# Optimization experiments

Measured on AMD Instinct MI355X. Metric: run time of the kernel, lower is better.

The kernel has to match this reference:

```python
import jax, jax.numpy as jnp
import numpy as np

B, S, C, H, D = 4, 2048, 512, 8, 64
EPS = 1e-5
SCALE = D ** -0.5


def layer_norm(x, w, b):
    m = jnp.mean(x, axis=-1, keepdims=True)
    v = jnp.var(x, axis=-1, keepdims=True)
    return (x - m) * jax.lax.rsqrt(v + EPS) * w + b


def setup_inputs() -> dict:
    key = jax.random.key(0)
    ks = jax.random.split(key, 7)
    s = 0.02
    return {
        "x": jax.random.normal(ks[0], (B, S, C), jnp.float32),
        "Wq": jax.random.normal(ks[1], (C, H * D), jnp.float32) * s,
        "Wk": jax.random.normal(ks[2], (C, H * D), jnp.float32) * s,
        "Wv": jax.random.normal(ks[3], (C, H * D), jnp.float32) * s,
        "Wo": jax.random.normal(ks[4], (H * D, C), jnp.float32) * s,
        "ln1_w": jnp.ones((C,), jnp.float32), "ln1_b": jnp.zeros((C,), jnp.float32),
        "ff_ln1_w": jnp.ones((C,), jnp.float32), "ff_ln1_b": jnp.zeros((C,), jnp.float32),
        "ff_w1": jax.random.normal(ks[5], (C, C), jnp.float32) * s, "ff_b1": jnp.zeros((C,), jnp.float32),
        "ff_ln2_w": jnp.ones((C,), jnp.float32), "ff_ln2_b": jnp.zeros((C,), jnp.float32),
        "ff_w2": jax.random.normal(ks[6], (C, C), jnp.float32) * s, "ff_b2": jnp.zeros((C,), jnp.float32),
        "ln2_w": jnp.ones((C,), jnp.float32), "ln2_b": jnp.zeros((C,), jnp.float32),
    }


def causal_attention(x, Wq, Wk, Wv, Wo):
    # Mathematically identical to the bucketed memory-efficient attention:
    # online-softmax bucketing changes compute order, not the result.
    q = (x @ Wq).reshape(B, S, H, D).transpose(0, 2, 1, 3)  # [B,H,S,D]
    k = (x @ Wk).reshape(B, S, H, D).transpose(0, 2, 1, 3)
    v = (x @ Wv).reshape(B, S, H, D).transpose(0, 2, 1, 3)
    scores = jnp.einsum('bhqd,bhkd->bhqk', q, k) * SCALE  # [B,H,S,S]
    causal = jnp.tril(jnp.ones((S, S), bool))
    scores = jnp.where(causal, scores, jnp.finfo(scores.dtype).min)
    attn = jax.nn.softmax(scores, axis=-1)
    out = jnp.einsum('bhqk,bhkd->bhqd', attn, v)
    out = out.transpose(0, 2, 1, 3).reshape(B, S, H * D)
    return out @ Wo


def reference(x, Wq, Wk, Wv, Wo, ln1_w, ln1_b, ff_ln1_w, ff_ln1_b, ff_w1, ff_b1,
              ff_ln2_w, ff_ln2_b, ff_w2, ff_b2, ln2_w, ln2_b):
    a = causal_attention(x, Wq, Wk, Wv, Wo)
    x_ln = layer_norm(a + x, ln1_w, ln1_b)
    h = layer_norm(x_ln, ff_ln1_w, ff_ln1_b) @ ff_w1 + ff_b1
    h = layer_norm(h, ff_ln2_w, ff_ln2_b) @ ff_w2 + ff_b2
    return layer_norm(h + x_ln, ln2_w, ln2_b)
```

## Files before the change

kernel.cpp:

```cpp
#include <hip/hip_runtime.h>

#define B_ 4
#define S_ 2048
#define C_ 512
#define H_ 8
#define D_ 64
#define M_ 8192

typedef short s8v __attribute__((ext_vector_type(8)));
typedef short s4v __attribute__((ext_vector_type(4)));
typedef float f4v __attribute__((ext_vector_type(4)));
typedef unsigned short u16;
typedef unsigned int u32;

__device__ __forceinline__ u16 f2b(float f) {
    u32 u = __builtin_bit_cast(u32, f);
    u = u + 0x7fffu + ((u >> 16) & 1u);
    return (u16)(u >> 16);
}

__device__ __forceinline__ void gl2lds16(const void* g, void* l) {
    __builtin_amdgcn_global_load_lds(
        (const __attribute__((address_space(1))) void*)g,
        (__attribute__((address_space(3))) void*)l, 16, 0, 0);
}

__global__ __launch_bounds__(256) void conv_k(const float* __restrict__ s,
                                              u16* __restrict__ d) {
    const int i = (blockIdx.x * 256 + threadIdx.x) * 4;
    const float4 v = *(const float4*)&s[i];
    ushort4 o;
    o.x = f2b(v.x); o.y = f2b(v.y); o.z = f2b(v.z); o.w = f2b(v.w);
    *(ushort4*)&d[i] = o;
}

__global__ __launch_bounds__(256) void trconv6_k(const float* __restrict__ s0,
                                                 const float* __restrict__ s1,
                                                 const float* __restrict__ s2,
                                                 const float* __restrict__ s3,
                                                 const float* __restrict__ s4,
                                                 const float* __restrict__ s5,
                                                 u16* __restrict__ d0,
                                                 u16* __restrict__ d1,
                                                 u16* __restrict__ d2,
                                                 u16* __restrict__ d3,
                                                 u16* __restrict__ d4,
                                                 u16* __restrict__ d5)
{
    const float* W; u16* Wt;
    switch (blockIdx.z) {
        case 0: W = s0; Wt = d0; break;
        case 1: W = s1; Wt = d1; break;
        case 2: W = s2; Wt = d2; break;
        case 3: W = s3; Wt = d3; break;
        case 4: W = s4; Wt = d4; break;
        default: W = s5; Wt = d5; break;
    }
    __shared__ float t[32][33];
    const int tx = threadIdx.x & 31, ty = threadIdx.x >> 5;
    const int n0 = blockIdx.x * 32, k0 = blockIdx.y * 32;
    #pragma unroll
    for (int i = 0; i < 4; ++i)
        t[ty + i * 8][tx] = W[(size_t)(k0 + ty + i * 8) * C_ + n0 + tx];
    __syncthreads();
    #pragma unroll
    for (int i = 0; i < 4; ++i)
        Wt[(size_t)(n0 + ty + i * 8) * C_ + k0 + tx] = f2b(t[tx][ty + i * 8]);
}

template <bool OB>
__global__ __launch_bounds__(256) void gemm_k(const u16* __restrict__ A,
                                              const u16* __restrict__ Bt,
                                              const float* __restrict__ bias,
                                              void* __restrict__ outv)
{
    __shared__ u16 As[2][4][16][32];
    __shared__ u16 Bs[2][4][16][32];
    const int tid = threadIdx.x;
    const int lane = tid & 63, w = tid >> 6;
    const int q4 = lane >> 4, l16 = lane & 15;
    const int wr = w >> 1, wc = w & 1;
    const int bm = blockIdx.y * 64, bn = blockIdx.x * 64;
    const int lr = lane >> 2, lc = (lane & 3) * 8;

    f4v acc[2][2];
    #pragma unroll
    for (int i = 0; i < 2; ++i)
        #pragma unroll
        for (int j = 0; j < 2; ++j) acc[i][j] = (f4v){0.f, 0.f, 0.f, 0.f};

    gl2lds16(A  + (size_t)(bm + w * 16 + lr) * C_ + lc, (char*)As + w * 1024);
    gl2lds16(Bt + (size_t)(bn + w * 16 + lr) * C_ + lc, (char*)Bs + w * 1024);

    for (int kt = 0; kt < 16; ++kt) {
        __syncthreads();
        const int buf = kt & 1;
        if (kt < 15) {
            const int nb = buf ^ 1, k0 = (kt + 1) * 32;
            gl2lds16(A  + (size_t)(bm + w * 16 + lr) * C_ + k0 + lc,
                     (char*)As + nb * 4096 + w * 1024);
            gl2lds16(Bt + (size_t)(bn + w * 16 + lr) * C_ + k0 + lc,
                     (char*)Bs + nb * 4096 + w * 1024);
        }
        s8v a[2], bfr[2];
        #pragma unroll
        for (int i = 0; i < 2; ++i) {
            const int row = wr * 32 + i * 16 + l16;
            a[i] = *(const s8v*)&As[buf][row >> 4][row & 15][q4 * 8];
        }
        #pragma unroll
        for (int j = 0; j < 2; ++j) {
            const int row = wc * 32 + j * 16 + l16;
            bfr[j] = *(const s8v*)&Bs[buf][row >> 4][row & 15][q4 * 8];
        }
        #pragma unroll
        for (int i = 0; i < 2; ++i)
            #pragma unroll
            for (int j = 0; j < 2; ++j)
                acc[i][j] = __builtin_amdgcn_mfma_f32_16x16x32_bf16(a[i], bfr[j], acc[i][j], 0, 0, 0);
    }

    #pragma unroll
    for (int j = 0; j < 2; ++j) {
        const int n = bn + wc * 32 + j * 16 + l16;
        const float bj = bias ? bias[n] : 0.0f;
        #pragma unroll
        for (int i = 0; i < 2; ++i) {
            const int m = bm + wr * 32 + i * 16 + q4 * 4;
            #pragma unroll
            for (int reg = 0; reg < 4; ++reg) {
                const float vv = acc[i][j][reg] + bj;
                if constexpr (OB) ((u16*)outv)[(size_t)(m + reg) * C_ + n] = f2b(vv);
                else              ((float*)outv)[(size_t)(m + reg) * C_ + n] = vv;
            }
        }
    }
}

__global__ __launch_bounds__(256) void qkv_k(const u16* __restrict__ A,
                                             const u16* __restrict__ Wq,
                                             const u16* __restrict__ Wk,
                                             const u16* __restrict__ Wv,
                                             u16* __restrict__ oq,
                                             u16* __restrict__ ok,
                                             u16* __restrict__ ovt)
{
    __shared__ u16 As[2][4][16][32];
    __shared__ u16 Bs[2][4][16][32];
    const int tid = threadIdx.x;
    const int lane = tid & 63, w = tid >> 6;
    const int q4 = lane >> 4, l16 = lane & 15;
    const int wr = w >> 1, wc = w & 1;
    const int nt = blockIdx.x, which = nt >> 3;
    const u16* Bt = which == 0 ? Wq : (which == 1 ? Wk : Wv);
    const int bm = blockIdx.y * 64, bn = (nt & 7) * 64;
    const int lr = lane >> 2, lc = (lane & 3) * 8;

    f4v acc[2][2];
    #pragma unroll
    for (int i = 0; i < 2; ++i)
        #pragma unroll
        for (int j = 0; j < 2; ++j) acc[i][j] = (f4v){0.f, 0.f, 0.f, 0.f};

    gl2lds16(A  + (size_t)(bm + w * 16 + lr) * C_ + lc, (char*)As + w * 1024);
    gl2lds16(Bt + (size_t)(bn + w * 16 + lr) * C_ + lc, (char*)Bs + w * 1024);

    for (int kt = 0; kt < 16; ++kt) {
        __syncthreads();
        const int buf = kt & 1;
        if (kt < 15) {
            const int nb = buf ^ 1, k0 = (kt + 1) * 32;
            gl2lds16(A  + (size_t)(bm + w * 16 + lr) * C_ + k0 + lc,
                     (char*)As + nb * 4096 + w * 1024);
            gl2lds16(Bt + (size_t)(bn + w * 16 + lr) * C_ + k0 + lc,
                     (char*)Bs + nb * 4096 + w * 1024);
        }
        s8v a[2], bfr[2];
        #pragma unroll
        for (int i = 0; i < 2; ++i) {
            const int row = wr * 32 + i * 16 + l16;
            a[i] = *(const s8v*)&As[buf][row >> 4][row & 15][q4 * 8];
        }
        #pragma unroll
        for (int j = 0; j < 2; ++j) {
            const int row = wc * 32 + j * 16 + l16;
            bfr[j] = *(const s8v*)&Bs[buf][row >> 4][row & 15][q4 * 8];
        }
        #pragma unroll
        for (int i = 0; i < 2; ++i)
            #pragma unroll
            for (int j = 0; j < 2; ++j)
                acc[i][j] = __builtin_amdgcn_mfma_f32_16x16x32_bf16(a[i], bfr[j], acc[i][j], 0, 0, 0);
    }

    if (which != 2) {
        u16* outp = which == 0 ? oq : ok;
        #pragma unroll
        for (int j = 0; j < 2; ++j) {
            const int n = bn + wc * 32 + j * 16 + l16;
            #pragma unroll
            for (int i = 0; i < 2; ++i) {
                const int m = bm + wr * 32 + i * 16 + q4 * 4;
                #pragma unroll
                for (int reg = 0; reg < 4; ++reg)
                    outp[(size_t)(m + reg) * C_ + n] = f2b(acc[i][j][reg]);
            }
        }
    } else {
        const int bglob = bm >> 11;
        const int sbase = bm & (S_ - 1);
        #pragma unroll
        for (int j = 0; j < 2; ++j) {
            const int n = bn + wc * 32 + j * 16 + l16;
            const int h = n >> 6, d = n & 63;
            u16* vrow = ovt + ((size_t)(bglob * H_ + h) * D_ + d) * S_;
            const int xw = d & 7;
            #pragma unroll
            for (int i = 0; i < 2; ++i) {
                const int s = sbase + wr * 32 + i * 16 + q4 * 4;
                const int pg = ((s & 31) >> 2) ^ xw;
                s4v pv;
                #pragma unroll
                for (int reg = 0; reg < 4; ++reg) pv[reg] = (short)f2b(acc[i][j][reg]);
                *(s4v*)&vrow[(s & ~31) + (pg << 2)] = pv;
            }
        }
    }
}

template <bool OB>
__global__ __launch_bounds__(256) void ln_k(const float* __restrict__ in,
                                            const float* __restrict__ res,
                                            const float* __restrict__ w,
                                            const float* __restrict__ bb,
                                            void* __restrict__ outv)
{
    const int lane = threadIdx.x & 63;
    const int row  = blockIdx.x * 4 + (threadIdx.x >> 6);
    const float* p = in + (size_t)row * C_;
    float4 v0 = *(const float4*)&p[lane * 4];
    float4 v1 = *(const float4*)&p[256 + lane * 4];
    if (res) {
        const float* rp = res + (size_t)row * C_;
        const float4 r0 = *(const float4*)&rp[lane * 4];
        const float4 r1 = *(const float4*)&rp[256 + lane * 4];
        v0.x += r0.x; v0.y += r0.y; v0.z += r0.z; v0.w += r0.w;
        v1.x += r1.x; v1.y += r1.y; v1.z += r1.z; v1.w += r1.w;
    }
    float s  = v0.x + v0.y + v0.z + v0.w + v1.x + v1.y + v1.z + v1.w;
    float ss = v0.x*v0.x + v0.y*v0.y + v0.z*v0.z + v0.w*v0.w
             + v1.x*v1.x + v1.y*v1.y + v1.z*v1.z + v1.w*v1.w;
    #pragma unroll
    for (int off = 32; off >= 1; off >>= 1) {
        s  += __shfl_xor(s, off);
        ss += __shfl_xor(ss, off);
    }
    const float mean = s * (1.0f / C_);
    const float var  = ss * (1.0f / C_) - mean * mean;
    const float rstd = rsqrtf(var + 1e-5f);

    const float4 w0 = *(const float4*)&w[lane * 4];
    const float4 w1 = *(const float4*)&w[256 + lane * 4];
    const float4 b0 = *(const float4*)&bb[lane * 4];
    const float4 b1 = *(const float4*)&bb[256 + lane * 4];
    float4 o0, o1;
    o0.x = (v0.x - mean) * rstd * w0.x + b0.x;
    o0.y = (v0.y - mean) * rstd * w0.y + b0.y;
    o0.z = (v0.z - mean) * rstd * w0.z + b0.z;
    o0.w = (v0.w - mean) * rstd * w0.w + b0.w;
    o1.x = (v1.x - mean) * rstd * w1.x + b1.x;
    o1.y = (v1.y - mean) * rstd * w1.y + b1.y;
    o1.z = (v1.z - mean) * rstd * w1.z + b1.z;
    o1.w = (v1.w - mean) * rstd * w1.w + b1.w;
    if constexpr (OB) {
        u16* op = (u16*)outv + (size_t)row * C_;
        ushort4 u0, u1;
        u0.x = f2b(o0.x); u0.y = f2b(o0.y); u0.z = f2b(o0.z); u0.w = f2b(o0.w);
        u1.x = f2b(o1.x); u1.y = f2b(o1.y); u1.z = f2b(o1.z); u1.w = f2b(o1.w);
        *(ushort4*)&op[lane * 4]       = u0;
        *(ushort4*)&op[256 + lane * 4] = u1;
    } else {
        float* op = (float*)outv + (size_t)row * C_;
        *(float4*)&op[lane * 4]       = o0;
        *(float4*)&op[256 + lane * 4] = o1;
    }
}

__global__ __launch_bounds__(256) void ln2x_k(const float* __restrict__ in,
                                              const float* __restrict__ res,
                                              const float* __restrict__ w1,
                                              const float* __restrict__ b1,
                                              const float* __restrict__ w2,
                                              const float* __restrict__ b2,
                                              float* __restrict__ out1,
                                              u16* __restrict__ out2)
{
    const int lane = threadIdx.x & 63;
    const int row  = blockIdx.x * 4 + (threadIdx.x >> 6);
    const float* p  = in  + (size_t)row * C_;
    const float* rp = res + (size_t)row * C_;
    float4 v0 = *(const float4*)&p[lane * 4];
    float4 v1 = *(const float4*)&p[256 + lane * 4];
    {
        const float4 r0 = *(const float4*)&rp[lane * 4];
        const float4 r1 = *(const float4*)&rp[256 + lane * 4];
        v0.x += r0.x; v0.y += r0.y; v0.z += r0.z; v0.w += r0.w;
        v1.x += r1.x; v1.y += r1.y; v1.z += r1.z; v1.w += r1.w;
    }
    float s  = v0.x + v0.y + v0.z + v0.w + v1.x + v1.y + v1.z + v1.w;
    float ss = v0.x*v0.x + v0.y*v0.y + v0.z*v0.z + v0.w*v0.w
             + v1.x*v1.x + v1.y*v1.y + v1.z*v1.z + v1.w*v1.w;
    #pragma unroll
    for (int off = 32; off >= 1; off >>= 1) {
        s  += __shfl_xor(s, off);
        ss += __shfl_xor(ss, off);
    }
    float mean = s * (1.0f / C_);
    float var  = ss * (1.0f / C_) - mean * mean;
    float rstd = rsqrtf(var + 1e-5f);

    const float4 wA0 = *(const float4*)&w1[lane * 4];
    const float4 wA1 = *(const float4*)&w1[256 + lane * 4];
    const float4 bA0 = *(const float4*)&b1[lane * 4];
    const float4 bA1 = *(const float4*)&b1[256 + lane * 4];
    float4 y0, y1v;
    y0.x  = (v0.x - mean) * rstd * wA0.x + bA0.x;
    y0.y  = (v0.y - mean) * rstd * wA0.y + bA0.y;
    y0.z  = (v0.z - mean) * rstd * wA0.z + bA0.z;
    y0.w  = (v0.w - mean) * rstd * wA0.w + bA0.w;
    y1v.x = (v1.x - mean) * rstd * wA1.x + bA1.x;
    y1v.y = (v1.y - mean) * rstd * wA1.y + bA1.y;
    y1v.z = (v1.z - mean) * rstd * wA1.z + bA1.z;
    y1v.w = (v1.w - mean) * rstd * wA1.w + bA1.w;
    float* op1 = out1 + (size_t)row * C_;
    *(float4*)&op1[lane * 4]       = y0;
    *(float4*)&op1[256 + lane * 4] = y1v;

    s  = y0.x + y0.y + y0.z + y0.w + y1v.x + y1v.y + y1v.z + y1v.w;
    ss = y0.x*y0.x + y0.y*y0.y + y0.z*y0.z + y0.w*y0.w
       + y1v.x*y1v.x + y1v.y*y1v.y + y1v.z*y1v.z + y1v.w*y1v.w;
    #pragma unroll
    for (int off = 32; off >= 1; off >>= 1) {
        s  += __shfl_xor(s, off);
        ss += __shfl_xor(ss, off);
    }
    mean = s * (1.0f / C_);
    var  = ss * (1.0f / C_) - mean * mean;
    rstd = rsqrtf(var + 1e-5f);

    const float4 wB0 = *(const float4*)&w2[lane * 4];
    const float4 wB1 = *(const float4*)&w2[256 + lane * 4];
    const float4 bB0 = *(const float4*)&b2[lane * 4];
    const float4 bB1 = *(const float4*)&b2[256 + lane * 4];
    ushort4 u0, u1;
    u0.x = f2b((y0.x - mean) * rstd * wB0.x + bB0.x);
    u0.y = f2b((y0.y - mean) * rstd * wB0.y + bB0.y);
    u0.z = f2b((y0.z - mean) * rstd * wB0.z + bB0.z);
    u0.w = f2b((y0.w - mean) * rstd * wB0.w + bB0.w);
    u1.x = f2b((y1v.x - mean) * rstd * wB1.x + bB1.x);
    u1.y = f2b((y1v.y - mean) * rstd * wB1.y + bB1.y);
    u1.z = f2b((y1v.z - mean) * rstd * wB1.z + bB1.z);
    u1.w = f2b((y1v.w - mean) * rstd * wB1.w + bB1.w);
    u16* op2 = out2 + (size_t)row * C_;
    *(ushort4*)&op2[lane * 4]       = u0;
    *(ushort4*)&op2[256 + lane * 4] = u1;
}

__global__ __launch_bounds__(256) void attn_k(const u16* __restrict__ Q,
                                              const u16* __restrict__ K,
                                              const u16* __restrict__ Vt,
                                              u16* __restrict__ O)
{
    __shared__ u16 Ks[2][2][64][32];
    __shared__ u16 Vs[2][2][64][32];
    const int tid = threadIdx.x;
    const int lane = tid & 63, w = tid >> 6;
    const int q4 = lane >> 4, l16 = lane & 15;
    const int x = blockIdx.x, h = blockIdx.y, b = blockIdx.z;
    const int qb = (x & 1) ? 31 - (x >> 1) : (x >> 1);
    const size_t base  = ((size_t)b * S_) * C_ + h * D_;
    const size_t basev = ((size_t)(b * H_ + h)) * D_ * S_;
    const int lr = lane >> 2, lc = (lane & 3) * 8;

    s8v qf[2];
    #pragma unroll
    for (int kh = 0; kh < 2; ++kh)
        qf[kh] = *(const s8v*)&Q[base + (size_t)(qb * 64 + w * 16 + l16) * C_ + kh * 32 + q4 * 8];

    #pragma unroll
    for (int r = 0; r < 2; ++r) {
        const int seg = r * 4 + w;
        const int row = (seg & 3) * 16 + lr;
        const int kh = seg >> 2;
        gl2lds16(K  + base  + (size_t)row * C_ + kh * 32 + lc, (char*)Ks + seg * 1024);
        gl2lds16(Vt + basev + (size_t)row * S_ + kh * 32 + lc, (char*)Vs + seg * 1024);
    }

    f4v o[4];
    float lp[4] = {0.f, 0.f, 0.f, 0.f};
    #pragma unroll
    for (int j = 0; j < 4; ++j) o[j] = (f4v){0.f, 0.f, 0.f, 0.f};

    const int qrow = w * 16 + l16;
    for (int kb = 0; kb <= qb; ++kb) {
        __syncthreads();
        const int buf = kb & 1;
        if (kb < qb) {
            const int nb = buf ^ 1, kn = kb + 1;
            #pragma unroll
            for (int r = 0; r < 2; ++r) {
                const int seg = r * 4 + w;
                const int row = (seg & 3) * 16 + lr;
                const int kh = seg >> 2;
                gl2lds16(K  + base  + (size_t)(kn * 64 + row) * C_ + kh * 32 + lc,
                         (char*)Ks + nb * 8192 + seg * 1024);
                gl2lds16(Vt + basev + (size_t)row * S_ + kn * 64 + kh * 32 + lc,
                         (char*)Vs + nb * 8192 + seg * 1024);
            }
        }

        f4v sc[4];
        #pragma unroll
        for (int j = 0; j < 4; ++j) sc[j] = (f4v){0.f, 0.f, 0.f, 0.f};
        #pragma unroll
        for (int kh = 0; kh < 2; ++kh) {
            #pragma unroll
            for (int j = 0; j < 4; ++j) {
                const s8v kf = *(const s8v*)&Ks[buf][kh][j * 16 + l16][q4 * 8];
                sc[j] = __builtin_amdgcn_mfma_f32_16x16x32_bf16(kf, qf[kh], sc[j], 0, 0, 0);
            }
        }

        const bool diag = (kb == qb);
        s4v pa[4];
        #pragma unroll
        for (int j = 0; j < 4; ++j) {
            float ps = 0.0f;
            #pragma unroll
            for (int reg = 0; reg < 4; ++reg) {
                float t = fmaf(sc[j][reg], 0.18033688011112043f, -11.541560327111707f);
                if (diag && (j * 16 + q4 * 4 + reg) > qrow) t = -128.0f;
                const float p = exp2f(t);
                ps += p;
                pa[j][reg] = (short)(__builtin_bit_cast(u32, p) >> 16);
            }
            lp[j] += ps;
        }

        #pragma unroll
        for (int c = 0; c < 4; ++c) {
            const int gh = (((c & 1) * 4 + q4) ^ (l16 & 7)) * 4;
            #pragma unroll
            for (int dj = 0; dj < 4; ++dj) {
                const s4v vb = *(const s4v*)&Vs[buf][c >> 1][dj * 16 + l16][gh];
                o[dj] = __builtin_amdgcn_mfma_f32_16x16x16bf16_1k(pa[c], vb, o[dj], 0, 0, 0);
            }
        }
    }

    float lt = (lp[0] + lp[1]) + (lp[2] + lp[3]);
    lt += __shfl_xor(lt, 16);
    lt += __shfl_xor(lt, 32);
    #pragma unroll
    for (int reg = 0; reg < 4; ++reg) {
        const float inv = 1.0f / __shfl(lt, q4 * 4 + reg);
        const size_t rowoff = base + (size_t)(qb * 64 + w * 16 + q4 * 4 + reg) * C_;
        #pragma unroll
        for (int dj = 0; dj < 4; ++dj)
            O[rowoff + dj * 16 + l16] = f2b(o[dj][reg] * inv);
    }
}

extern "C" void kernel_launch(void* const* d_in, const int* in_sizes, int n_in,
                              void* d_out, int out_size, void* d_ws, size_t ws_size,
                              hipStream_t stream)
{
    const float* x       = (const float*)d_in[0];
    const float* Wq      = (const float*)d_in[1];
    const float* Wk      = (const float*)d_in[2];
    const float* Wv      = (const float*)d_in[3];
    const float* Wo      = (const float*)d_in[4];
    const float* ln1_w   = (const float*)d_in[5];
    const float* ln1_b   = (const float*)d_in[6];
    const float* ffln1_w = (const float*)d_in[7];
    const float* ffln1_b = (const float*)d_in[8];
    const float* ff_w1   = (const float*)d_in[9];
    const float* ff_b1   = (const float*)d_in[10];
    const float* ffln2_w = (const float*)d_in[11];
    const float* ffln2_b = (const float*)d_in[12];
    const float* ff_w2   = (const float*)d_in[13];
    const float* ff_b2   = (const float*)d_in[14];
    const float* ln2_w   = (const float*)d_in[15];
    const float* ln2_b   = (const float*)d_in[16];
    float* out = (float*)d_out;

    const size_t MC = (size_t)M_ * C_;
    const size_t WW = (size_t)C_ * C_;
    u16* xb   = (u16*)d_ws;
    u16* WqT  = xb + MC;
    u16* WkT  = WqT + WW;
    u16* WvT  = WkT + WW;
    u16* WoT  = WvT + WW;
    u16* W1T  = WoT + WW;
    u16* W2T  = W1T + WW;
    u16* qbuf = W2T + WW;
    u16* kbuf = qbuf + MC;
    u16* vbuf = kbuf + MC;
    u16* vtbuf= vbuf + MC;
    u16*  abuf = xb;
    float* tf  = (float*)qbuf;
    float* xln = (float*)vbuf;

    const dim3 gg(C_ / 64, M_ / 64);
    const dim3 gq(24, M_ / 64);
    const dim3 ga(32, H_, B_);
    const dim3 gt(16, 16, 6);
    const int  gl = M_ / 4;

    conv_k<<<MC / 1024, 256, 0, stream>>>(x, xb);
    trconv6_k<<<gt, 256, 0, stream>>>(Wq, Wk, Wv, Wo, ff_w1, ff_w2,
                                      WqT, WkT, WvT, WoT, W1T, W2T);

    qkv_k<<<gq, 256, 0, stream>>>(xb, WqT, WkT, WvT, qbuf, kbuf, vtbuf);
    attn_k<<<ga, 256, 0, stream>>>(qbuf, kbuf, vtbuf, abuf);

    gemm_k<false><<<gg, 256, 0, stream>>>(abuf, WoT, nullptr, tf);
    ln2x_k<<<gl, 256, 0, stream>>>(tf, x, ln1_w, ln1_b, ffln1_w, ffln1_b,
                                   xln, xb);
    gemm_k<false><<<gg, 256, 0, stream>>>(xb, W1T, ff_b1, tf);
    ln_k<true><<<gl, 256, 0, stream>>>(tf, nullptr, ffln2_w, ffln2_b, xb);
    gemm_k<false><<<gg, 256, 0, stream>>>(xb, W2T, ff_b2, tf);
    ln_k<false><<<gl, 256, 0, stream>>>(tf, xln, ln2_w, ln2_b, out);
}
```

Measured before the change: 267.6 us.

## Store GEMM and LayerNorm intermediates in bf16 and swizzle K layout

```diff
diff --git a/kernel.cpp b/kernel.cpp
--- a/kernel.cpp
+++ b/kernel.cpp
@@ -17,6 +17,12 @@
     u32 u = __builtin_bit_cast(u32, f);
     u = u + 0x7fffu + ((u >> 16) & 1u);
     return (u16)(u >> 16);
+}
+
+__device__ __forceinline__ void b2f8(const s8v v, float* f) {
+    #pragma unroll
+    for (int k = 0; k < 8; ++k)
+        f[k] = __builtin_bit_cast(float, (u32)(u16)v[k] << 16);
 }
 
 __device__ __forceinline__ void gl2lds16(const void* g, void* l) {
@@ -193,8 +199,7 @@
                 acc[i][j] = __builtin_amdgcn_mfma_f32_16x16x32_bf16(a[i], bfr[j], acc[i][j], 0, 0, 0);
     }
 
-    if (which != 2) {
-        u16* outp = which == 0 ? oq : ok;
+    if (which == 0) {
         #pragma unroll
         for (int j = 0; j < 2; ++j) {
             const int n = bn + wc * 32 + j * 16 + l16;
@@ -203,7 +208,20 @@
                 const int m = bm + wr * 32 + i * 16 + q4 * 4;
                 #pragma unroll
                 for (int reg = 0; reg < 4; ++reg)
-                    outp[(size_t)(m + reg) * C_ + n] = f2b(acc[i][j][reg]);
+                    oq[(size_t)(m + reg) * C_ + n] = f2b(acc[i][j][reg]);
+            }
+        }
+    } else if (which == 1) {
+        #pragma unroll
+        for (int j = 0; j < 2; ++j) {
+            const int n = bn + wc * 32 + j * 16 + l16;
+            const int nswz = (n & ~31) | ((((n >> 3) & 3) ^ q4) << 3) | (n & 7);
+            #pragma unroll
+            for (int i = 0; i < 2; ++i) {
+                const int m = bm + wr * 32 + i * 16 + q4 * 4;
+                #pragma unroll
+                for (int reg = 0; reg < 4; ++reg)
+                    ok[(size_t)(m + reg) * C_ + nswz] = f2b(acc[i][j][reg]);
             }
         }
     } else {
@@ -228,142 +246,138 @@
     }
 }
 
-template <bool OB>
-__global__ __launch_bounds__(256) void ln_k(const float* __restrict__ in,
-                                            const float* __restrict__ res,
-                                            const float* __restrict__ w,
-                                            const float* __restrict__ bb,
-                                            void* __restrict__ outv)
+__global__ __launch_bounds__(256) void ln2xb_k(const u16* __restrict__ in,
+                                               const float* __restrict__ res,
+                                               const float* __restrict__ w1,
+                                               const float* __restrict__ b1,
+                                               const float* __restrict__ w2,
+                                               const float* __restrict__ b2,
+                                               u16* __restrict__ out1,
+                                               u16* __restrict__ out2)
 {
     const int lane = threadIdx.x & 63;
     const int row  = blockIdx.x * 4 + (threadIdx.x >> 6);
-    const float* p = in + (size_t)row * C_;
-    float4 v0 = *(const float4*)&p[lane * 4];
-    float4 v1 = *(const float4*)&p[256 + lane * 4];
-    if (res) {
-        const float* rp = res + (size_t)row * C_;
-        const float4 r0 = *(const float4*)&rp[lane * 4];
-        const float4 r1 = *(const float4*)&rp[256 + lane * 4];
-        v0.x += r0.x; v0.y += r0.y; v0.z += r0.z; v0.w += r0.w;
-        v1.x += r1.x; v1.y += r1.y; v1.z += r1.z; v1.w += r1.w;
-    }
-    float s  = v0.x + v0.y + v0.z + v0.w + v1.x + v1.y + v1.z + v1.w;
-    float ss = v0.x*v0.x + v0.y*v0.y + v0.z*v0.z + v0.w*v0.w
-             + v1.x*v1.x + v1.y*v1.y + v1.z*v1.z + v1.w*v1.w;
-    #pragma unroll
-    for (int off = 32; off >= 1; off >>= 1) {
-        s  += __shfl_xor(s, off);
-        ss += __shfl_xor(ss, off);
-    }
-    const float mean = s * (1.0f / C_);
-    const float var  = ss * (1.0f / C_) - mean * mean;
-    const float rstd = rsqrtf(var + 1e-5f);
-
-    const float4 w0 = *(const float4*)&w[lane * 4];
-    const float4 w1 = *(const float4*)&w[256 + lane * 4];
-    const float4 b0 = *(const float4*)&bb[lane * 4];
-    const float4 b1 = *(const float4*)&bb[256 + lane * 4];
-    float4 o0, o1;
-    o0.x = (v0.x - mean) * rstd * w0.x + b0.x;
-    o0.y = (v0.y - mean) * rstd * w0.y + b0.y;
-    o0.z = (v0.z - mean) * rstd * w0.z + b0.z;
-    o0.w = (v0.w - mean) * rstd * w0.w + b0.w;
-    o1.x = (v1.x - mean) * rstd * w1.x + b1.x;
-    o1.y = (v1.y - mean) * rstd * w1.y + b1.y;
-    o1.z = (v1.z - mean) * rstd * w1.z + b1.z;
-    o1.w = (v1.w - mean) * rstd * w1.w + b1.w;
-    if constexpr (OB) {
-        u16* op = (u16*)outv + (size_t)row * C_;
-        ushort4 u0, u1;
-        u0.x = f2b(o0.x); u0.y = f2b(o0.y); u0.z = f2b(o0.z); u0.w = f2b(o0.w);
-        u1.x = f2b(o1.x); u1.y = f2b(o1.y); u1.z = f2b(o1.z); u1.w = f2b(o1.w);
-        *(ushort4*)&op[lane * 4]       = u0;
-        *(ushort4*)&op[256 + lane * 4] = u1;
-    } else {
-        float* op = (float*)outv + (size_t)row * C_;
-        *(float4*)&op[lane * 4]       = o0;
-        *(float4*)&op[256 + lane * 4] = o1;
-    }
-}
-
-__global__ __launch_bounds__(256) void ln2x_k(const float* __restrict__ in,
-                                              const float* __restrict__ res,
-                                              const float* __restrict__ w1,
-                                              const float* __restrict__ b1,
-                                              const float* __restrict__ w2,
-                                              const float* __restrict__ b2,
-                                              float* __restrict__ out1,
-                                              u16* __restrict__ out2)
+    const size_t off = (size_t)row * C_ + lane * 8;
+    float v[8];
+    b2f8(*(const s8v*)&in[off], v);
+    {
+        const float4 r0 = *(const float4*)&res[off];
+        const float4 r1 = *(const float4*)&res[off + 4];
+        v[0] += r0.x; v[1] += r0.y; v[2] += r0.z; v[3] += r0.w;
+        v[4] += r1.x; v[5] += r1.y; v[6] += r1.z; v[7] += r1.w;
+    }
+    float s = 0.f, ss = 0.f;
+    #pragma unroll
+    for (int k = 0; k < 8; ++k) { s += v[k]; ss += v[k] * v[k]; }
+    #pragma unroll
+    for (int o = 32; o >= 1; o >>= 1) { s += __shfl_xor(s, o); ss += __shfl_xor(ss, o); }
+    float mean = s * (1.0f / C_);
+    float rstd = rsqrtf(ss * (1.0f / C_) - mean * mean + 1e-5f);
+
+    const float4 wA0 = *(const float4*)&w1[lane * 8];
+    const float4 wA1 = *(const float4*)&w1[lane * 8 + 4];
+    const float4 bA0 = *(const float4*)&b1[lane * 8];
+    const float4 bA1 = *(const float4*)&b1[lane * 8 + 4];
+    const float wA[8] = {wA0.x, wA0.y, wA0.z, wA0.w, wA1.x, wA1.y, wA1.z, wA1.w};
+    const float bA[8] = {bA0.x, bA0.y, bA0.z, bA0.w, bA1.x, bA1.y, bA1.z, bA1.w};
+    float y[8];
+    s8v o1;
+    #pragma unroll
+    for (int k = 0; k < 8; ++k) {
+        y[k] = (v[k] - mean) * rstd * wA[k] + bA[k];
+        o1[k] = (short)f2b(y[k]);
+    }
+    *(s8v*)&out1[off] = o1;
+
+    s = 0.f; ss = 0.f;
+    #pragma unroll
+    for (int k = 0; k < 8; ++k) { s += y[k]; ss += y[k] * y[k]; }
+    #pragma unroll
+    for (int o = 32; o >= 1; o >>= 1) { s += __shfl_xor(s, o); ss += __shfl_xor(ss, o); }
+    mean = s * (1.0f / C_);
+    rstd = rsqrtf(ss * (1.0f / C_) - mean * mean + 1e-5f);
+
+    const float4 wB0 = *(const float4*)&w2[lane * 8];
+    const float4 wB1 = *(const float4*)&w2[lane * 8 + 4];
+    const float4 bB0 = *(const float4*)&b2[lane * 8];
+    const float4 bB1 = *(const float4*)&b2[lane * 8 + 4];
+    const float wB[8] = {wB0.x, wB0.y, wB0.z, wB0.w, wB1.x, wB1.y, wB1.z, wB1.w};
+    const float bB[8] = {bB0.x, bB0.y, bB0.z, bB0.w, bB1.x, bB1.y, bB1.z, bB1.w};
+    s8v o2;
+    #pragma unroll
+    for (int k = 0; k < 8; ++k)
+        o2[k] = (short)f2b((y[k] - mean) * rstd * wB[k] + bB[k]);
+    *(s8v*)&out2[off] = o2;
+}
+
+__global__ __launch_bounds__(256) void lnb_k(const u16* __restrict__ in,
+                                             const float* __restrict__ w,
+                                             const float* __restrict__ bb,
+                                             u16* __restrict__ out)
 {
     const int lane = threadIdx.x & 63;
     const int row  = blockIdx.x * 4 + (threadIdx.x >> 6);
-    const float* p  = in  + (size_t)row * C_;
-    const float* rp = res + (size_t)row * C_;
-    float4 v0 = *(const float4*)&p[lane * 4];
-    float4 v1 = *(const float4*)&p[256 + lane * 4];
-    {
-        const float4 r0 = *(const float4*)&rp[lane * 4];
-        const float4 r1 = *(const float4*)&rp[256 + lane * 4];
-        v0.x += r0.x; v0.y += r0.y; v0.z += r0.z; v0.w += r0.w;
-        v1.x += r1.x; v1.y += r1.y; v1.z += r1.z; v1.w += r1.w;
-    }
-    float s  = v0.x + v0.y + v0.z + v0.w + v1.x + v1.y + v1.z + v1.w;
-    float ss = v0.x*v0.x + v0.y*v0.y + v0.z*v0.z + v0.w*v0.w
-             + v1.x*v1.x + v1.y*v1.y + v1.z*v1.z + v1.w*v1.w;
-    #pragma unroll
-    for (int off = 32; off >= 1; off >>= 1) {
-        s  += __shfl_xor(s, off);
-        ss += __shfl_xor(ss, off);
-    }
-    float mean = s * (1.0f / C_);
-    float var  = ss * (1.0f / C_) - mean * mean;
-    float rstd = rsqrtf(var + 1e-5f);
-
-    const float4 wA0 = *(const float4*)&w1[lane * 4];
-    const float4 wA1 = *(const float4*)&w1[256 + lane * 4];
-    const float4 bA0 = *(const float4*)&b1[lane * 4];
-    const float4 bA1 = *(const float4*)&b1[256 + lane * 4];
-    float4 y0, y1v;
-    y0.x  = (v0.x - mean) * rstd * wA0.x + bA0.x;
-    y0.y  = (v0.y - mean) * rstd * wA0.y + bA0.y;
-    y0.z  = (v0.z - mean) * rstd * wA0.z + bA0.z;
-    y0.w  = (v0.w - mean) * rstd * wA0.w + bA0.w;
-    y1v.x = (v1.x - mean) * rstd * wA1.x + bA1.x;
-    y1v.y = (v1.y - mean) * rstd * wA1.y + bA1.y;
-    y1v.z = (v1.z - mean) * rstd * wA1.z + bA1.z;
-    y1v.w = (v1.w - mean) * rstd * wA1.w + bA1.w;
-    float* op1 = out1 + (size_t)row * C_;
-    *(float4*)&op1[lane * 4]       = y0;
-    *(float4*)&op1[256 + lane * 4] = y1v;
-
-    s  = y0.x + y0.y + y0.z + y0.w + y1v.x + y1v.y + y1v.z + y1v.w;
-    ss = y0.x*y0.x + y0.y*y0.y + y0.z*y0.z + y0.w*y0.w
-       + y1v.x*y1v.x + y1v.y*y1v.y + y1v.z*y1v.z + y1v.w*y1v.w;
-    #pragma unroll
-    for (int off = 32; off >= 1; off >>= 1) {
-        s  += __shfl_xor(s, off);
-        ss += __shfl_xor(ss, off);
-    }
-    mean = s * (1.0f / C_);
-    var  = ss * (1.0f / C_) - mean * mean;
-    rstd = rsqrtf(var + 1e-5f);
-
-    const float4 wB0 = *(const float4*)&w2[lane * 4];
-    const float4 wB1 = *(const float4*)&w2[256 + lane * 4];
-    const float4 bB0 = *(const float4*)&b2[lane * 4];
-    const float4 bB1 = *(const float4*)&b2[256 + lane * 4];
-    ushort4 u0, u1;
-    u0.x = f2b((y0.x - mean) * rstd * wB0.x + bB0.x);
-    u0.y = f2b((y0.y - mean) * rstd * wB0.y + bB0.y);
-    u0.z = f2b((y0.z - mean) * rstd * wB0.z + bB0.z);
-    u0.w = f2b((y0.w - mean) * rstd * wB0.w + bB0.w);
-    u1.x = f2b((y1v.x - mean) * rstd * wB1.x + bB1.x);
-    u1.y = f2b((y1v.y - mean) * rstd * wB1.y + bB1.y);
-    u1.z = f2b((y1v.z - mean) * rstd * wB1.z + bB1.z);
-    u1.w = f2b((y1v.w - mean) * rstd * wB1.w + bB1.w);
-    u16* op2 = out2 + (size_t)row * C_;
-    *(ushort4*)&op2[lane * 4]       = u0;
-    *(ushort4*)&op2[256 + lane * 4] = u1;
+    const size_t off = (size_t)row * C_ + lane * 8;
+    float v[8];
+    b2f8(*(const s8v*)&in[off], v);
+    float s = 0.f, ss = 0.f;
+    #pragma unroll
+    for (int k = 0; k < 8; ++k) { s += v[k]; ss += v[k] * v[k]; }
+    #pragma unroll
+    for (int o = 32; o >= 1; o >>= 1) { s += __shfl_xor(s, o); ss += __shfl_xor(ss, o); }
+    const float mean = s * (1.0f / C_);
+    const float rstd = rsqrtf(ss * (1.0f / C_) - mean * mean + 1e-5f);
+    const float4 w0 = *(const float4*)&w[lane * 8];
+    const float4 w1 = *(const float4*)&w[lane * 8 + 4];
+    const float4 b0 = *(const float4*)&bb[lane * 8];
+    const float4 b1 = *(const float4*)&bb[lane * 8 + 4];
+    const float wv[8] = {w0.x, w0.y, w0.z, w0.w, w1.x, w1.y, w1.z, w1.w};
+    const float bv[8] = {b0.x, b0.y, b0.z, b0.w, b1.x, b1.y, b1.z, b1.w};
+    s8v o;
+    #pragma unroll
+    for (int k = 0; k < 8; ++k)
+        o[k] = (short)f2b((v[k] - mean) * rstd * wv[k] + bv[k]);
+    *(s8v*)&out[off] = o;
+}
+
+__global__ __launch_bounds__(256) void lnfin_k(const u16* __restrict__ in,
+                                               const u16* __restrict__ res,
+                                               const float* __restrict__ w,
+                                               const float* __restrict__ bb,
+                                               float* __restrict__ out)
+{
+    const int lane = threadIdx.x & 63;
+    const int row  = blockIdx.x * 4 + (threadIdx.x >> 6);
+    const size_t off = (size_t)row * C_ + lane * 8;
+    float v[8], r[8];
+    b2f8(*(const s8v*)&in[off], v);
+    b2f8(*(const s8v*)&res[off], r);
+    #pragma unroll
+    for (int k = 0; k < 8; ++k) v[k] += r[k];
+    float s = 0.f, ss = 0.f;
+    #pragma unroll
+    for (int k = 0; k < 8; ++k) { s += v[k]; ss += v[k] * v[k]; }
+    #pragma unroll
+    for (int o = 32; o >= 1; o >>= 1) { s += __shfl_xor(s, o); ss += __shfl_xor(ss, o); }
+    const float mean = s * (1.0f / C_);
+    const float rstd = rsqrtf(ss * (1.0f / C_) - mean * mean + 1e-5f);
+    const float4 w0 = *(const float4*)&w[lane * 8];
+    const float4 w1 = *(const float4*)&w[lane * 8 + 4];
+    const float4 b0 = *(const float4*)&bb[lane * 8];
+    const float4 b1 = *(const float4*)&bb[lane * 8 + 4];
+    const float wv[8] = {w0.x, w0.y, w0.z, w0.w, w1.x, w1.y, w1.z, w1.w};
+    const float bv[8] = {b0.x, b0.y, b0.z, b0.w, b1.x, b1.y, b1.z, b1.w};
+    float4 o0, o1;
+    o0.x = (v[0] - mean) * rstd * wv[0] + bv[0];
+    o0.y = (v[1] - mean) * rstd * wv[1] + bv[1];
+    o0.z = (v[2] - mean) * rstd * wv[2] + bv[2];
+    o0.w = (v[3] - mean) * rstd * wv[3] + bv[3];
+    o1.x = (v[4] - mean) * rstd * wv[4] + bv[4];
+    o1.y = (v[5] - mean) * rstd * wv[5] + bv[5];
+    o1.z = (v[6] - mean) * rstd * wv[6] + bv[6];
+    o1.w = (v[7] - mean) * rstd * wv[7] + bv[7];
+    *(float4*)&out[off]     = o0;
+    *(float4*)&out[off + 4] = o1;
 }
 
 __global__ __launch_bounds__(256) void attn_k(const u16* __restrict__ Q,
@@ -381,6 +395,7 @@
     const size_t base  = ((size_t)b * S_) * C_ + h * D_;
     const size_t basev = ((size_t)(b * H_ + h)) * D_ * S_;
     const int lr = lane >> 2, lc = (lane & 3) * 8;
+    const int kq = (q4 ^ ((l16 >> 2) & 3)) * 8;
 
     s8v qf[2];
     #pragma unroll
@@ -426,7 +441,7 @@
         for (int kh = 0; kh < 2; ++kh) {
             #pragma unroll
             for (int j = 0; j < 4; ++j) {
-                const s8v kf = *(const s8v*)&Ks[buf][kh][j * 16 + l16][q4 * 8];
+                const s8v kf = *(const s8v*)&Ks[buf][kh][j * 16 + l16][kq];
                 sc[j] = __builtin_amdgcn_mfma_f32_16x16x32_bf16(kf, qf[kh], sc[j], 0, 0, 0);
             }
         }
@@ -508,8 +523,8 @@
     u16* vbuf = kbuf + MC;
     u16* vtbuf= vbuf + MC;
     u16*  abuf = xb;
-    float* tf  = (float*)qbuf;
-    float* xln = (float*)vbuf;
+    u16*  tf   = qbuf;
+    u16*  xln  = vbuf;
 
     const dim3 gg(C_ / 64, M_ / 64);
     const dim3 gq(24, M_ / 64);
@@ -524,11 +539,11 @@
     qkv_k<<<gq, 256, 0, stream>>>(xb, WqT, WkT, WvT, qbuf, kbuf, vtbuf);
     attn_k<<<ga, 256, 0, stream>>>(qbuf, kbuf, vtbuf, abuf);
 
-    gemm_k<false><<<gg, 256, 0, stream>>>(abuf, WoT, nullptr, tf);
-    ln2x_k<<<gl, 256, 0, stream>>>(tf, x, ln1_w, ln1_b, ffln1_w, ffln1_b,
-                                   xln, xb);
-    gemm_k<false><<<gg, 256, 0, stream>>>(xb, W1T, ff_b1, tf);
-    ln_k<true><<<gl, 256, 0, stream>>>(tf, nullptr, ffln2_w, ffln2_b, xb);
-    gemm_k<false><<<gg, 256, 0, stream>>>(xb, W2T, ff_b2, tf);
-    ln_k<false><<<gl, 256, 0, stream>>>(tf, xln, ln2_w, ln2_b, out);
-}
+    gemm_k<true><<<gg, 256, 0, stream>>>(abuf, WoT, nullptr, tf);
+    ln2xb_k<<<gl, 256, 0, stream>>>(tf, x, ln1_w, ln1_b, ffln1_w, ffln1_b,
+                                    xln, xb);
+    gemm_k<true><<<gg, 256, 0, stream>>>(xb, W1T, ff_b1, tf);
+    lnb_k<<<gl, 256, 0, stream>>>(tf, ffln2_w, ffln2_b, xb);
+    gemm_k<true><<<gg, 256, 0, stream>>>(xb, W2T, ff_b2, tf);
+    lnfin_k<<<gl, 256, 0, stream>>>(tf, xln, ln2_w, ln2_b, out);
+}
```

Result: no change. 263.5 us (-1.5%).
